# Optimization experiments

Hardware: AMD Instinct MI355X
Metric: run time of the kernel (lower is better)

Reference implementation:

```python
import jax, jax.numpy as jnp
import numpy as np

GROUP_SIZE = 128
TOP_K = 2
ZERO_POINT = 8  # Marlin symmetric zero point: w = scale * (q - 8)


def _dequant_int4(q, scales, group_size):
    # q: [E, N, K] int values in [0,15]; scales: [E, N, K//group_size]
    s = jnp.repeat(scales, group_size, axis=-1)  # [E, N, K]
    return (q.astype(jnp.float32) - float(ZERO_POINT)) * s


def setup_inputs() -> dict:
    key = jax.random.key(0)
    k1, k2, k3, k4, k5, k6 = jax.random.split(key, 6)
    B, S, H, I, E = 2, 1024, 2048, 1408, 8
    router_logits = jax.random.normal(k1, (B, S, E), dtype=jnp.float32)
    hidden_states = jax.random.normal(k2, (B, S, H), dtype=jnp.float32)
    fc_gate_up_qweights = jax.random.randint(k3, (E, 2 * I, H), 0, 16, dtype=jnp.int32)
    fc_gate_up_scales = jax.random.uniform(k4, (E, 2 * I, H // GROUP_SIZE), dtype=jnp.float32) * 0.02
    fc_down_qweights = jax.random.randint(k5, (E, H, I), 0, 16, dtype=jnp.int32)
    fc_down_scales = jax.random.uniform(k6, (E, H, I // GROUP_SIZE), dtype=jnp.float32) * 0.02
    return {
        "router_logits": router_logits,
        "hidden_states": hidden_states,
        "fc_gate_up_qweights": fc_gate_up_qweights,
        "fc_gate_up_scales": fc_gate_up_scales,
        "fc_down_qweights": fc_down_qweights,
        "fc_down_scales": fc_down_scales,
    }


def reference(router_logits, hidden_states, fc_gate_up_qweights, fc_gate_up_scales,
              fc_down_qweights, fc_down_scales):
    B, S, H = hidden_states.shape
    E = router_logits.shape[-1]
    T = B * S
    x = hidden_states.reshape(T, H)
    logits = router_logits.reshape(T, E)

    # top-k routing with softmax over selected logits
    top_vals, top_idx = jax.lax.top_k(logits, TOP_K)          # [T, k]
    top_w = jax.nn.softmax(top_vals, axis=-1)                 # [T, k]
    route_w = jnp.zeros((T, E), x.dtype).at[jnp.arange(T)[:, None], top_idx].set(top_w)  # [T, E]

    # dequantize int4 weights: scale * (q - 8), per-group along K
    w_gate_up = _dequant_int4(fc_gate_up_qweights, fc_gate_up_scales, GROUP_SIZE)  # [E, 2I, H]
    w_down = _dequant_int4(fc_down_qweights, fc_down_scales, GROUP_SIZE)          # [E, H, I]

    # grouped GEMM (dense over experts, masked by routing weights)
    gu = jnp.einsum('th,enh->ten', x, w_gate_up)              # [T, E, 2I]
    gate, up = jnp.split(gu, 2, axis=-1)
    act = jax.nn.silu(gate) * up                              # SwiGLU, [T, E, I]
    out = jnp.einsum('tei,ehi,te->th', act, w_down, route_w)  # [T, H]
    return out.reshape(B, S, H)
```

## Files before the change

### kernel.cpp

```cpp
#include <hip/hip_runtime.h>
#include <hip/hip_bf16.h>

#define T_TOKENS 2048
#define H_DIM    2048
#define I_DIM    1408
#define E_NUM    8

typedef __bf16 bf16;
typedef __attribute__((ext_vector_type(4))) __bf16  bf16x4;
typedef __attribute__((ext_vector_type(8))) __bf16  bf16x8;
typedef __attribute__((ext_vector_type(4))) float   floatx4;

static const size_t OFF_COUNTS = 0;
static const size_t OFF_LISTS  = 256;
static const size_t OFF_WLISTS = OFF_LISTS + (size_t)T_TOKENS * E_NUM * 4;
static const size_t OFF_ACT    = 262144;
static const size_t OFF_TMP    = OFF_ACT + (size_t)2 * T_TOKENS * I_DIM * 2;

__global__ void router_kernel(const float* __restrict__ logits,
                              int* __restrict__ counts,
                              int* __restrict__ lists,
                              float* __restrict__ wlists)
{
    int t = blockIdx.x * blockDim.x + threadIdx.x;
    if (t >= T_TOKENS) return;
    const float* l = logits + (size_t)t * E_NUM;
    float v0 = -1e30f, v1 = -1e30f;
    int i0 = 0, i1 = 0;
    #pragma unroll
    for (int e = 0; e < E_NUM; ++e) {
        float v = l[e];
        if (v > v0) { v1 = v0; i1 = i0; v0 = v; i0 = e; }
        else if (v > v1) { v1 = v; i1 = e; }
    }
    float w0 = 1.f / (1.f + __expf(v1 - v0));
    float w1 = 1.f - w0;
    int p0 = atomicAdd(&counts[i0], 1);
    lists[i0 * T_TOKENS + p0] = t * 2 + 0;
    wlists[i0 * T_TOKENS + p0] = w0;
    int p1 = atomicAdd(&counts[i1], 1);
    lists[i1 * T_TOKENS + p1] = t * 2 + 1;
    wlists[i1 * T_TOKENS + p1] = w1;
}

__global__ __launch_bounds__(256) void gemm1_kernel(
    const float* __restrict__ x,
    const int*   __restrict__ qw,
    const float* __restrict__ sc,
    const int*   __restrict__ counts,
    const int*   __restrict__ lists,
    bf16*        __restrict__ act)
{
    const int e   = blockIdx.z;
    const int cnt = counts[e];
    const int m0  = blockIdx.y * 128;
    if (m0 >= cnt) return;
    const int n0 = blockIdx.x * 64;

    __shared__ __align__(16) bf16 Al[128 * 64];
    __shared__ __align__(16) bf16 Bl[128 * 64];
    __shared__ int meta[128];

    const int tid = threadIdx.x;
    if (tid < 128) {
        int m = m0 + tid;
        meta[tid] = lists[e * T_TOKENS + (m < cnt ? m : 0)];
    }
    __syncthreads();

    const int lane = tid & 63;
    const int wv = tid >> 6;
    const int wm = wv >> 1, wn = wv & 1;

    floatx4 acc[4][4];
    #pragma unroll
    for (int i = 0; i < 4; ++i)
        #pragma unroll
        for (int j = 0; j < 4; ++j)
            acc[i][j] = (floatx4){0.f, 0.f, 0.f, 0.f};

    const int srow = tid >> 4;
    const int scol = (tid & 15) * 4;

    for (int k0 = 0; k0 < H_DIM; k0 += 64) {
        #pragma unroll
        for (int it = 0; it < 8; ++it) {
            int r = srow + 16 * it;
            int tok = meta[r] >> 1;
            float4 v = *reinterpret_cast<const float4*>(x + (size_t)tok * H_DIM + k0 + scol);
            bf16x4 bv; bv.x = (bf16)v.x; bv.y = (bf16)v.y; bv.z = (bf16)v.z; bv.w = (bf16)v.w;
            *reinterpret_cast<bf16x4*>(&Al[r * 64 + scol]) = bv;
        }
        #pragma unroll
        for (int it = 0; it < 8; ++it) {
            int r = srow + 16 * it;
            int tt = r >> 4, within = r & 15;
            int grow = ((tt & 1) ? I_DIM : 0) + n0 + (tt >> 1) * 16 + within;
            const int4 q = *reinterpret_cast<const int4*>(qw + (size_t)(e * 2816 + grow) * H_DIM + k0 + scol);
            float s = sc[(e * 2816 + grow) * 16 + (k0 >> 7)];
            bf16x4 bv;
            bv.x = (bf16)((float)(q.x - 8) * s);
            bv.y = (bf16)((float)(q.y - 8) * s);
            bv.z = (bf16)((float)(q.z - 8) * s);
            bv.w = (bf16)((float)(q.w - 8) * s);
            *reinterpret_cast<bf16x4*>(&Bl[r * 64 + scol]) = bv;
        }
        __syncthreads();
        #pragma unroll
        for (int ks = 0; ks < 2; ++ks) {
            const int kofs = ks * 32 + (lane >> 4) * 8;
            bf16x8 af[4], bfr[4];
            #pragma unroll
            for (int mt = 0; mt < 4; ++mt)
                af[mt] = *reinterpret_cast<const bf16x8*>(&Al[(wm * 64 + mt * 16 + (lane & 15)) * 64 + kofs]);
            #pragma unroll
            for (int nt = 0; nt < 4; ++nt)
                bfr[nt] = *reinterpret_cast<const bf16x8*>(&Bl[(wn * 64 + nt * 16 + (lane & 15)) * 64 + kofs]);
            #pragma unroll
            for (int mt = 0; mt < 4; ++mt)
                #pragma unroll
                for (int nt = 0; nt < 4; ++nt)
                    acc[mt][nt] = __builtin_amdgcn_mfma_f32_16x16x32_bf16(af[mt], bfr[nt], acc[mt][nt], 0, 0, 0);
        }
        __syncthreads();
    }

    const int rbase = (lane >> 4) * 4;
    const int cn = lane & 15;
    #pragma unroll
    for (int mt = 0; mt < 4; ++mt) {
        #pragma unroll
        for (int j = 0; j < 2; ++j) {
            floatx4 g = acc[mt][2 * j];
            floatx4 u = acc[mt][2 * j + 1];
            int col = n0 + wn * 32 + j * 16 + cn;
            #pragma unroll
            for (int r = 0; r < 4; ++r) {
                int lrow = wm * 64 + mt * 16 + rbase + r;
                if (m0 + lrow < cnt) {
                    float gate = g[r], up = u[r];
                    float a = gate / (1.f + __expf(-gate)) * up;
                    act[(size_t)meta[lrow] * I_DIM + col] = (bf16)a;
                }
            }
        }
    }
}

__global__ __launch_bounds__(256) void gemm2_kernel(
    const bf16*  __restrict__ act,
    const int*   __restrict__ qw,
    const float* __restrict__ sc,
    const int*   __restrict__ counts,
    const int*   __restrict__ lists,
    const float* __restrict__ wlists,
    float*       __restrict__ tmp)
{
    const int e   = blockIdx.z;
    const int cnt = counts[e];
    const int m0  = blockIdx.y * 128;
    if (m0 >= cnt) return;
    const int n0 = blockIdx.x * 128;

    __shared__ __align__(16) bf16 Al[128 * 64];
    __shared__ __align__(16) bf16 Bl[128 * 64];
    __shared__ int   meta[128];
    __shared__ float wmeta[128];

    const int tid = threadIdx.x;
    if (tid < 128) {
        int m = m0 + tid;
        int mm = (m < cnt) ? m : 0;
        meta[tid]  = lists[e * T_TOKENS + mm];
        wmeta[tid] = wlists[e * T_TOKENS + mm];
    }
    __syncthreads();

    const int lane = tid & 63;
    const int wv = tid >> 6;
    const int wm = wv >> 1, wn = wv & 1;

    floatx4 acc[4][4];
    #pragma unroll
    for (int i = 0; i < 4; ++i)
        #pragma unroll
        for (int j = 0; j < 4; ++j)
            acc[i][j] = (floatx4){0.f, 0.f, 0.f, 0.f};

    const int srow = tid >> 4;
    const int scol = (tid & 15) * 4;

    for (int k0 = 0; k0 < I_DIM; k0 += 64) {
        #pragma unroll
        for (int it = 0; it < 8; ++it) {
            int r = srow + 16 * it;
            bf16x4 v = *reinterpret_cast<const bf16x4*>(act + (size_t)meta[r] * I_DIM + k0 + scol);
            *reinterpret_cast<bf16x4*>(&Al[r * 64 + scol]) = v;
        }
        #pragma unroll
        for (int it = 0; it < 8; ++it) {
            int r = srow + 16 * it;
            int grow = n0 + r;
            const int4 q = *reinterpret_cast<const int4*>(qw + (size_t)(e * H_DIM + grow) * I_DIM + k0 + scol);
            float s = sc[(e * H_DIM + grow) * 11 + (k0 >> 7)];
            bf16x4 bv;
            bv.x = (bf16)((float)(q.x - 8) * s);
            bv.y = (bf16)((float)(q.y - 8) * s);
            bv.z = (bf16)((float)(q.z - 8) * s);
            bv.w = (bf16)((float)(q.w - 8) * s);
            *reinterpret_cast<bf16x4*>(&Bl[r * 64 + scol]) = bv;
        }
        __syncthreads();
        #pragma unroll
        for (int ks = 0; ks < 2; ++ks) {
            const int kofs = ks * 32 + (lane >> 4) * 8;
            bf16x8 af[4], bfr[4];
            #pragma unroll
            for (int mt = 0; mt < 4; ++mt)
                af[mt] = *reinterpret_cast<const bf16x8*>(&Al[(wm * 64 + mt * 16 + (lane & 15)) * 64 + kofs]);
            #pragma unroll
            for (int nt = 0; nt < 4; ++nt)
                bfr[nt] = *reinterpret_cast<const bf16x8*>(&Bl[(wn * 64 + nt * 16 + (lane & 15)) * 64 + kofs]);
            #pragma unroll
            for (int mt = 0; mt < 4; ++mt)
                #pragma unroll
                for (int nt = 0; nt < 4; ++nt)
                    acc[mt][nt] = __builtin_amdgcn_mfma_f32_16x16x32_bf16(af[mt], bfr[nt], acc[mt][nt], 0, 0, 0);
        }
        __syncthreads();
    }

    const int rbase = (lane >> 4) * 4;
    const int cn = lane & 15;
    #pragma unroll
    for (int mt = 0; mt < 4; ++mt) {
        #pragma unroll
        for (int nt = 0; nt < 4; ++nt) {
            floatx4 v = acc[mt][nt];
            int col = n0 + wn * 64 + nt * 16 + cn;
            #pragma unroll
            for (int r = 0; r < 4; ++r) {
                int lrow = wm * 64 + mt * 16 + rbase + r;
                if (m0 + lrow < cnt) {
                    tmp[(size_t)meta[lrow] * H_DIM + col] = wmeta[lrow] * v[r];
                }
            }
        }
    }
}

__global__ void finalize_kernel(const float* __restrict__ tmp, float* __restrict__ out)
{
    int i4 = blockIdx.x * blockDim.x + threadIdx.x;
    int t  = i4 >> 9;
    int h  = (i4 & 511) * 4;
    float4 a = *reinterpret_cast<const float4*>(tmp + ((size_t)2 * t) * H_DIM + h);
    float4 b = *reinterpret_cast<const float4*>(tmp + ((size_t)(2 * t + 1)) * H_DIM + h);
    float4 o;
    o.x = a.x + b.x; o.y = a.y + b.y; o.z = a.z + b.z; o.w = a.w + b.w;
    *reinterpret_cast<float4*>(out + (size_t)t * H_DIM + h) = o;
}

extern "C" void kernel_launch(void* const* d_in, const int* in_sizes, int n_in,
                              void* d_out, int out_size, void* d_ws, size_t ws_size,
                              hipStream_t stream)
{
    const float* router_logits = (const float*)d_in[0];
    const float* x             = (const float*)d_in[1];
    const int*   gu_q          = (const int*)d_in[2];
    const float* gu_s          = (const float*)d_in[3];
    const int*   dn_q          = (const int*)d_in[4];
    const float* dn_s          = (const float*)d_in[5];
    float* out = (float*)d_out;

    char* ws = (char*)d_ws;
    int*   counts = (int*)(ws + OFF_COUNTS);
    int*   lists  = (int*)(ws + OFF_LISTS);
    float* wlists = (float*)(ws + OFF_WLISTS);
    bf16*  act    = (bf16*)(ws + OFF_ACT);
    float* tmp    = (float*)(ws + OFF_TMP);

    hipMemsetAsync(counts, 0, E_NUM * sizeof(int), stream);
    router_kernel<<<T_TOKENS / 256, 256, 0, stream>>>(router_logits, counts, lists, wlists);
    gemm1_kernel<<<dim3(22, 16, 8), 256, 0, stream>>>(x, gu_q, gu_s, counts, lists, act);
    gemm2_kernel<<<dim3(16, 16, 8), 256, 0, stream>>>(act, dn_q, dn_s, counts, lists, wlists, tmp);
    finalize_kernel<<<4096, 256, 0, stream>>>(tmp, out);
}
```

Baseline: 559.6 us.

## Pre-pack int4 weights to nibbles, pre-convert x to bf16, atomic-add output

Adds per-call pre-pass kernels that pack the int32 quantized weights into 4-bit nibbles and convert hidden states to bf16. The GEMMs then load the packed words and dequantize them with an FMA per element, and load activations with wider 16-byte vector loads. The finalize kernel and tmp buffer are removed: gemm2 atomically adds weighted results straight into a zeroed output. The pack kernels still read all int32 weights every call, so total traffic may not drop, and the fp32 atomics make the summation order nondeterministic.

```diff
diff --git a/kernel.cpp b/kernel.cpp
--- a/kernel.cpp
+++ b/kernel.cpp
@@ -14,8 +14,38 @@
 static const size_t OFF_COUNTS = 0;
 static const size_t OFF_LISTS  = 256;
 static const size_t OFF_WLISTS = OFF_LISTS + (size_t)T_TOKENS * E_NUM * 4;
-static const size_t OFF_ACT    = 262144;
-static const size_t OFF_TMP    = OFF_ACT + (size_t)2 * T_TOKENS * I_DIM * 2;
+static const size_t OFF_XB     = 131328;
+static const size_t OFF_ACT    = OFF_XB + (size_t)T_TOKENS * H_DIM * 2;
+static const size_t OFF_GUPK   = OFF_ACT + (size_t)2 * T_TOKENS * I_DIM * 2;
+static const size_t OFF_DNPK   = OFF_GUPK + (size_t)E_NUM * 2 * I_DIM * (H_DIM / 8) * 4;
+
+__global__ void pack_nib_kernel(const int* __restrict__ q, uint2* __restrict__ out, int n2)
+{
+    int i = blockIdx.x * blockDim.x + threadIdx.x;
+    if (i >= n2) return;
+    const int4* q4 = reinterpret_cast<const int4*>(q) + (size_t)i * 4;
+    int4 a = q4[0], b = q4[1], c = q4[2], d = q4[3];
+    unsigned d0 = (unsigned)(a.x & 15) | ((unsigned)(a.y & 15) << 4) |
+                  ((unsigned)(a.z & 15) << 8) | ((unsigned)(a.w & 15) << 12) |
+                  ((unsigned)(b.x & 15) << 16) | ((unsigned)(b.y & 15) << 20) |
+                  ((unsigned)(b.z & 15) << 24) | ((unsigned)(b.w & 15) << 28);
+    unsigned d1 = (unsigned)(c.x & 15) | ((unsigned)(c.y & 15) << 4) |
+                  ((unsigned)(c.z & 15) << 8) | ((unsigned)(c.w & 15) << 12) |
+                  ((unsigned)(d.x & 15) << 16) | ((unsigned)(d.y & 15) << 20) |
+                  ((unsigned)(d.z & 15) << 24) | ((unsigned)(d.w & 15) << 28);
+    out[i] = make_uint2(d0, d1);
+}
+
+__global__ void xconv_kernel(const float* __restrict__ x, bf16* __restrict__ xb)
+{
+    int i = blockIdx.x * blockDim.x + threadIdx.x;
+    const float4* x4 = reinterpret_cast<const float4*>(x) + (size_t)i * 2;
+    float4 v0 = x4[0], v1 = x4[1];
+    bf16x8 bv;
+    bv[0] = (bf16)v0.x; bv[1] = (bf16)v0.y; bv[2] = (bf16)v0.z; bv[3] = (bf16)v0.w;
+    bv[4] = (bf16)v1.x; bv[5] = (bf16)v1.y; bv[6] = (bf16)v1.z; bv[7] = (bf16)v1.w;
+    *reinterpret_cast<bf16x8*>(xb + (size_t)i * 8) = bv;
+}
 
 __global__ void router_kernel(const float* __restrict__ logits,
                               int* __restrict__ counts,
@@ -44,12 +74,12 @@
 }
 
 __global__ __launch_bounds__(256) void gemm1_kernel(
-    const float* __restrict__ x,
-    const int*   __restrict__ qw,
-    const float* __restrict__ sc,
-    const int*   __restrict__ counts,
-    const int*   __restrict__ lists,
-    bf16*        __restrict__ act)
+    const bf16*     __restrict__ xb,
+    const unsigned* __restrict__ qpk,
+    const float*    __restrict__ sc,
+    const int*      __restrict__ counts,
+    const int*      __restrict__ lists,
+    bf16*           __restrict__ act)
 {
     const int e   = blockIdx.z;
     const int cnt = counts[e];
@@ -79,31 +109,32 @@
         for (int j = 0; j < 4; ++j)
             acc[i][j] = (floatx4){0.f, 0.f, 0.f, 0.f};
 
-    const int srow = tid >> 4;
-    const int scol = (tid & 15) * 4;
+    const int kg   = tid & 7;
+    const int rb   = tid >> 3;
 
     for (int k0 = 0; k0 < H_DIM; k0 += 64) {
         #pragma unroll
-        for (int it = 0; it < 8; ++it) {
-            int r = srow + 16 * it;
-            int tok = meta[r] >> 1;
-            float4 v = *reinterpret_cast<const float4*>(x + (size_t)tok * H_DIM + k0 + scol);
-            bf16x4 bv; bv.x = (bf16)v.x; bv.y = (bf16)v.y; bv.z = (bf16)v.z; bv.w = (bf16)v.w;
-            *reinterpret_cast<bf16x4*>(&Al[r * 64 + scol]) = bv;
-        }
-        #pragma unroll
-        for (int it = 0; it < 8; ++it) {
-            int r = srow + 16 * it;
+        for (int j = 0; j < 4; ++j) {
+            int g = tid + 256 * j;
+            int row = g >> 3, cg = g & 7;
+            int tok = meta[row] >> 1;
+            bf16x8 v = *reinterpret_cast<const bf16x8*>(xb + (size_t)tok * H_DIM + k0 + cg * 8);
+            *reinterpret_cast<bf16x8*>(&Al[g * 8]) = v;
+        }
+        #pragma unroll
+        for (int j = 0; j < 4; ++j) {
+            int r = rb + 32 * j;
             int tt = r >> 4, within = r & 15;
             int grow = ((tt & 1) ? I_DIM : 0) + n0 + (tt >> 1) * 16 + within;
-            const int4 q = *reinterpret_cast<const int4*>(qw + (size_t)(e * 2816 + grow) * H_DIM + k0 + scol);
-            float s = sc[(e * 2816 + grow) * 16 + (k0 >> 7)];
-            bf16x4 bv;
-            bv.x = (bf16)((float)(q.x - 8) * s);
-            bv.y = (bf16)((float)(q.y - 8) * s);
-            bv.z = (bf16)((float)(q.z - 8) * s);
-            bv.w = (bf16)((float)(q.w - 8) * s);
-            *reinterpret_cast<bf16x4*>(&Bl[r * 64 + scol]) = bv;
+            size_t rbase = (size_t)(e * 2816 + grow);
+            unsigned pd = qpk[rbase * 256 + (k0 >> 3) + kg];
+            float s = sc[rbase * 16 + (k0 >> 7)];
+            float m8s = -8.f * s;
+            bf16x8 bv;
+            #pragma unroll
+            for (int jj = 0; jj < 8; ++jj)
+                bv[jj] = (bf16)fmaf((float)((pd >> (4 * jj)) & 15u), s, m8s);
+            *reinterpret_cast<bf16x8*>(&Bl[r * 64 + kg * 8]) = bv;
         }
         __syncthreads();
         #pragma unroll
@@ -148,13 +179,13 @@
 }
 
 __global__ __launch_bounds__(256) void gemm2_kernel(
-    const bf16*  __restrict__ act,
-    const int*   __restrict__ qw,
-    const float* __restrict__ sc,
-    const int*   __restrict__ counts,
-    const int*   __restrict__ lists,
-    const float* __restrict__ wlists,
-    float*       __restrict__ tmp)
+    const bf16*     __restrict__ act,
+    const unsigned* __restrict__ qpk,
+    const float*    __restrict__ sc,
+    const int*      __restrict__ counts,
+    const int*      __restrict__ lists,
+    const float*    __restrict__ wlists,
+    float*          __restrict__ out)
 {
     const int e   = blockIdx.z;
     const int cnt = counts[e];
@@ -187,28 +218,30 @@
         for (int j = 0; j < 4; ++j)
             acc[i][j] = (floatx4){0.f, 0.f, 0.f, 0.f};
 
-    const int srow = tid >> 4;
-    const int scol = (tid & 15) * 4;
+    const int kg = tid & 7;
+    const int rb = tid >> 3;
 
     for (int k0 = 0; k0 < I_DIM; k0 += 64) {
         #pragma unroll
-        for (int it = 0; it < 8; ++it) {
-            int r = srow + 16 * it;
-            bf16x4 v = *reinterpret_cast<const bf16x4*>(act + (size_t)meta[r] * I_DIM + k0 + scol);
-            *reinterpret_cast<bf16x4*>(&Al[r * 64 + scol]) = v;
-        }
-        #pragma unroll
-        for (int it = 0; it < 8; ++it) {
-            int r = srow + 16 * it;
+        for (int j = 0; j < 4; ++j) {
+            int g = tid + 256 * j;
+            int row = g >> 3, cg = g & 7;
+            bf16x8 v = *reinterpret_cast<const bf16x8*>(act + (size_t)meta[row] * I_DIM + k0 + cg * 8);
+            *reinterpret_cast<bf16x8*>(&Al[g * 8]) = v;
+        }
+        #pragma unroll
+        for (int j = 0; j < 4; ++j) {
+            int r = rb + 32 * j;
             int grow = n0 + r;
-            const int4 q = *reinterpret_cast<const int4*>(qw + (size_t)(e * H_DIM + grow) * I_DIM + k0 + scol);
-            float s = sc[(e * H_DIM + grow) * 11 + (k0 >> 7)];
-            bf16x4 bv;
-            bv.x = (bf16)((float)(q.x - 8) * s);
-            bv.y = (bf16)((float)(q.y - 8) * s);
-            bv.z = (bf16)((float)(q.z - 8) * s);
-            bv.w = (bf16)((float)(q.w - 8) * s);
-            *reinterpret_cast<bf16x4*>(&Bl[r * 64 + scol]) = bv;
+            size_t rbase = (size_t)(e * H_DIM + grow);
+            unsigned pd = qpk[rbase * 176 + (k0 >> 3) + kg];
+            float s = sc[rbase * 11 + (k0 >> 7)];
+            float m8s = -8.f * s;
+            bf16x8 bv;
+            #pragma unroll
+            for (int jj = 0; jj < 8; ++jj)
+                bv[jj] = (bf16)fmaf((float)((pd >> (4 * jj)) & 15u), s, m8s);
+            *reinterpret_cast<bf16x8*>(&Bl[r * 64 + kg * 8]) = bv;
         }
         __syncthreads();
         #pragma unroll
@@ -242,23 +275,12 @@
             for (int r = 0; r < 4; ++r) {
                 int lrow = wm * 64 + mt * 16 + rbase + r;
                 if (m0 + lrow < cnt) {
-                    tmp[(size_t)meta[lrow] * H_DIM + col] = wmeta[lrow] * v[r];
+                    int tok = meta[lrow] >> 1;
+                    unsafeAtomicAdd(&out[(size_t)tok * H_DIM + col], wmeta[lrow] * v[r]);
                 }
             }
         }
     }
-}
-
-__global__ void finalize_kernel(const float* __restrict__ tmp, float* __restrict__ out)
-{
-    int i4 = blockIdx.x * blockDim.x + threadIdx.x;
-    int t  = i4 >> 9;
-    int h  = (i4 & 511) * 4;
-    float4 a = *reinterpret_cast<const float4*>(tmp + ((size_t)2 * t) * H_DIM + h);
-    float4 b = *reinterpret_cast<const float4*>(tmp + ((size_t)(2 * t + 1)) * H_DIM + h);
-    float4 o;
-    o.x = a.x + b.x; o.y = a.y + b.y; o.z = a.z + b.z; o.w = a.w + b.w;
-    *reinterpret_cast<float4*>(out + (size_t)t * H_DIM + h) = o;
 }
 
 extern "C" void kernel_launch(void* const* d_in, const int* in_sizes, int n_in,
@@ -274,15 +296,24 @@
     float* out = (float*)d_out;
 
     char* ws = (char*)d_ws;
-    int*   counts = (int*)(ws + OFF_COUNTS);
-    int*   lists  = (int*)(ws + OFF_LISTS);
-    float* wlists = (float*)(ws + OFF_WLISTS);
-    bf16*  act    = (bf16*)(ws + OFF_ACT);
-    float* tmp    = (float*)(ws + OFF_TMP);
+    int*      counts = (int*)(ws + OFF_COUNTS);
+    int*      lists  = (int*)(ws + OFF_LISTS);
+    float*    wlists = (float*)(ws + OFF_WLISTS);
+    bf16*     xb     = (bf16*)(ws + OFF_XB);
+    bf16*     act    = (bf16*)(ws + OFF_ACT);
+    unsigned* gu_pk  = (unsigned*)(ws + OFF_GUPK);
+    unsigned* dn_pk  = (unsigned*)(ws + OFF_DNPK);
 
     hipMemsetAsync(counts, 0, E_NUM * sizeof(int), stream);
+    hipMemsetAsync(out, 0, (size_t)out_size * sizeof(float), stream);
+
+    const int n2_gu = E_NUM * 2 * I_DIM * H_DIM / 16;
+    const int n2_dn = E_NUM * H_DIM * I_DIM / 16;
+    pack_nib_kernel<<<(n2_gu + 255) / 256, 256, 0, stream>>>(gu_q, (uint2*)gu_pk, n2_gu);
+    pack_nib_kernel<<<(n2_dn + 255) / 256, 256, 0, stream>>>(dn_q, (uint2*)dn_pk, n2_dn);
+    xconv_kernel<<<T_TOKENS * H_DIM / 8 / 256, 256, 0, stream>>>(x, xb);
+
     router_kernel<<<T_TOKENS / 256, 256, 0, stream>>>(router_logits, counts, lists, wlists);
-    gemm1_kernel<<<dim3(22, 16, 8), 256, 0, stream>>>(x, gu_q, gu_s, counts, lists, act);
-    gemm2_kernel<<<dim3(16, 16, 8), 256, 0, stream>>>(act, dn_q, dn_s, counts, lists, wlists, tmp);
-    finalize_kernel<<<4096, 256, 0, stream>>>(tmp, out);
-}
+    gemm1_kernel<<<dim3(22, 16, 8), 256, 0, stream>>>(xb, gu_pk, gu_s, counts, lists, act);
+    gemm2_kernel<<<dim3(16, 16, 8), 256, 0, stream>>>(act, dn_pk, dn_s, counts, lists, wlists, out);
+}
```

After: 568.7 us. About the same (+1.6%).

## Pre-dequantize weights into swizzled bf16 tiles and pre-convert activations

Applied to the files above, without the earlier changes.

Adds pack kernels that dequantize the int4-as-int32 weights once into bf16, laid out tile-contiguous with an XOR swizzle, plus a kernel that converts x to bf16. The GEMM kernels then do plain 16-byte copies into shared memory with conflict-free swizzled fragment reads. The aim is to stop re-reading fp32/int32 data and re-dequantizing it once per M-tile, and to cut LDS bank conflicts. The cost is extra full passes over the weights each call (read int32, write bf16) and a larger workspace, with tmp now overlapping the gate-up packed buffer.

```diff
diff --git a/kernel.cpp b/kernel.cpp
--- a/kernel.cpp
+++ b/kernel.cpp
@@ -7,15 +7,85 @@
 #define E_NUM    8
 
 typedef __bf16 bf16;
-typedef __attribute__((ext_vector_type(4))) __bf16  bf16x4;
 typedef __attribute__((ext_vector_type(8))) __bf16  bf16x8;
 typedef __attribute__((ext_vector_type(4))) float   floatx4;
 
 static const size_t OFF_COUNTS = 0;
 static const size_t OFF_LISTS  = 256;
 static const size_t OFF_WLISTS = OFF_LISTS + (size_t)T_TOKENS * E_NUM * 4;
-static const size_t OFF_ACT    = 262144;
-static const size_t OFF_TMP    = OFF_ACT + (size_t)2 * T_TOKENS * I_DIM * 2;
+static const size_t OFF_XB     = 131328;
+static const size_t OFF_ACT    = OFF_XB + (size_t)T_TOKENS * H_DIM * 2;
+static const size_t OFF_GUPK   = OFF_ACT + (size_t)2 * T_TOKENS * I_DIM * 2;
+static const size_t OFF_DNPK   = OFF_GUPK + (size_t)E_NUM * 22 * 32 * 16384;
+static const size_t OFF_TMP    = OFF_GUPK;
+
+__global__ __launch_bounds__(256) void pack_gu_kernel(const int* __restrict__ q,
+                                                      const float* __restrict__ sc,
+                                                      bf16* __restrict__ out)
+{
+    const int b = blockIdx.x;
+    const int t = threadIdx.x;
+    const int e = b / 2816;
+    const int grow = b - e * 2816;
+    const int4* qp = reinterpret_cast<const int4*>(q + (size_t)b * H_DIM) + t * 2;
+    int4 a = qp[0], c = qp[1];
+    float s = sc[(size_t)b * 16 + (t >> 4)];
+    float m8s = -8.f * s;
+    bf16x8 bv;
+    bv[0] = (bf16)fmaf((float)a.x, s, m8s);
+    bv[1] = (bf16)fmaf((float)a.y, s, m8s);
+    bv[2] = (bf16)fmaf((float)a.z, s, m8s);
+    bv[3] = (bf16)fmaf((float)a.w, s, m8s);
+    bv[4] = (bf16)fmaf((float)c.x, s, m8s);
+    bv[5] = (bf16)fmaf((float)c.y, s, m8s);
+    bv[6] = (bf16)fmaf((float)c.z, s, m8s);
+    bv[7] = (bf16)fmaf((float)c.w, s, m8s);
+    const int is_up = grow >= I_DIM;
+    const int icol  = grow - (is_up ? I_DIM : 0);
+    const int nt    = icol >> 6;
+    const int r     = ((((icol >> 4) & 3) * 2 + is_up) * 16) + (icol & 15);
+    size_t dst = ((((size_t)e * 22 + nt) * 32 + (t >> 3)) * 128 + r) * 8 + ((t & 7) ^ (r & 7));
+    reinterpret_cast<bf16x8*>(out)[dst] = bv;
+}
+
+__global__ __launch_bounds__(256) void pack_dn_kernel(const int* __restrict__ q,
+                                                      const float* __restrict__ sc,
+                                                      bf16* __restrict__ out)
+{
+    const int b = blockIdx.x;
+    const int t = threadIdx.x;
+    if (t >= 176) return;
+    const int e = b >> 11;
+    const int grow = b & 2047;
+    const int4* qp = reinterpret_cast<const int4*>(q + (size_t)b * I_DIM) + t * 2;
+    int4 a = qp[0], c = qp[1];
+    float s = sc[(size_t)b * 11 + (t >> 4)];
+    float m8s = -8.f * s;
+    bf16x8 bv;
+    bv[0] = (bf16)fmaf((float)a.x, s, m8s);
+    bv[1] = (bf16)fmaf((float)a.y, s, m8s);
+    bv[2] = (bf16)fmaf((float)a.z, s, m8s);
+    bv[3] = (bf16)fmaf((float)a.w, s, m8s);
+    bv[4] = (bf16)fmaf((float)c.x, s, m8s);
+    bv[5] = (bf16)fmaf((float)c.y, s, m8s);
+    bv[6] = (bf16)fmaf((float)c.z, s, m8s);
+    bv[7] = (bf16)fmaf((float)c.w, s, m8s);
+    const int nt = grow >> 7;
+    const int r  = grow & 127;
+    size_t dst = ((((size_t)e * 16 + nt) * 22 + (t >> 3)) * 128 + r) * 8 + ((t & 7) ^ (r & 7));
+    reinterpret_cast<bf16x8*>(out)[dst] = bv;
+}
+
+__global__ void xconv_kernel(const float* __restrict__ x, bf16* __restrict__ xb)
+{
+    int i = blockIdx.x * blockDim.x + threadIdx.x;
+    const float4* x4 = reinterpret_cast<const float4*>(x) + (size_t)i * 2;
+    float4 v0 = x4[0], v1 = x4[1];
+    bf16x8 bv;
+    bv[0] = (bf16)v0.x; bv[1] = (bf16)v0.y; bv[2] = (bf16)v0.z; bv[3] = (bf16)v0.w;
+    bv[4] = (bf16)v1.x; bv[5] = (bf16)v1.y; bv[6] = (bf16)v1.z; bv[7] = (bf16)v1.w;
+    *reinterpret_cast<bf16x8*>(xb + (size_t)i * 8) = bv;
+}
 
 __global__ void router_kernel(const float* __restrict__ logits,
                               int* __restrict__ counts,
@@ -44,21 +114,20 @@
 }
 
 __global__ __launch_bounds__(256) void gemm1_kernel(
-    const float* __restrict__ x,
-    const int*   __restrict__ qw,
-    const float* __restrict__ sc,
-    const int*   __restrict__ counts,
-    const int*   __restrict__ lists,
-    bf16*        __restrict__ act)
+    const bf16* __restrict__ xb,
+    const bf16* __restrict__ wpk,
+    const int*  __restrict__ counts,
+    const int*  __restrict__ lists,
+    bf16*       __restrict__ act)
 {
     const int e   = blockIdx.z;
     const int cnt = counts[e];
     const int m0  = blockIdx.y * 128;
     if (m0 >= cnt) return;
-    const int n0 = blockIdx.x * 64;
-
-    __shared__ __align__(16) bf16 Al[128 * 64];
-    __shared__ __align__(16) bf16 Bl[128 * 64];
+    const int nt  = blockIdx.x;
+
+    __shared__ __align__(16) bf16 Al[8192];
+    __shared__ __align__(16) bf16 Bl[8192];
     __shared__ int meta[128];
 
     const int tid = threadIdx.x;
@@ -72,6 +141,30 @@
     const int wv = tid >> 6;
     const int wm = wv >> 1, wn = wv & 1;
 
+    int    aoff[4];
+    size_t agbl[4];
+    #pragma unroll
+    for (int j = 0; j < 4; ++j) {
+        int g = tid + 256 * j;
+        int arow = g >> 3, cg = g & 7;
+        aoff[j] = arow * 64 + ((cg ^ (arow & 7)) * 8);
+        agbl[j] = (size_t)(meta[arow] >> 1) * H_DIM + cg * 8;
+    }
+    const bf16* bt = wpk + ((size_t)e * 22 + nt) * (32 * 8192) + tid * 8;
+
+    int afr[2][4], bfr[2][4];
+    #pragma unroll
+    for (int ks = 0; ks < 2; ++ks) {
+        int gidx = ks * 4 + (lane >> 4);
+        #pragma unroll
+        for (int t4 = 0; t4 < 4; ++t4) {
+            int ra = wm * 64 + t4 * 16 + (lane & 15);
+            afr[ks][t4] = ra * 64 + ((gidx ^ (ra & 7)) * 8);
+            int rb = wn * 64 + t4 * 16 + (lane & 15);
+            bfr[ks][t4] = rb * 64 + ((gidx ^ (rb & 7)) * 8);
+        }
+    }
+
     floatx4 acc[4][4];
     #pragma unroll
     for (int i = 0; i < 4; ++i)
@@ -79,48 +172,33 @@
         for (int j = 0; j < 4; ++j)
             acc[i][j] = (floatx4){0.f, 0.f, 0.f, 0.f};
 
-    const int srow = tid >> 4;
-    const int scol = (tid & 15) * 4;
-
     for (int k0 = 0; k0 < H_DIM; k0 += 64) {
         #pragma unroll
-        for (int it = 0; it < 8; ++it) {
-            int r = srow + 16 * it;
-            int tok = meta[r] >> 1;
-            float4 v = *reinterpret_cast<const float4*>(x + (size_t)tok * H_DIM + k0 + scol);
-            bf16x4 bv; bv.x = (bf16)v.x; bv.y = (bf16)v.y; bv.z = (bf16)v.z; bv.w = (bf16)v.w;
-            *reinterpret_cast<bf16x4*>(&Al[r * 64 + scol]) = bv;
-        }
-        #pragma unroll
-        for (int it = 0; it < 8; ++it) {
-            int r = srow + 16 * it;
-            int tt = r >> 4, within = r & 15;
-            int grow = ((tt & 1) ? I_DIM : 0) + n0 + (tt >> 1) * 16 + within;
-            const int4 q = *reinterpret_cast<const int4*>(qw + (size_t)(e * 2816 + grow) * H_DIM + k0 + scol);
-            float s = sc[(e * 2816 + grow) * 16 + (k0 >> 7)];
-            bf16x4 bv;
-            bv.x = (bf16)((float)(q.x - 8) * s);
-            bv.y = (bf16)((float)(q.y - 8) * s);
-            bv.z = (bf16)((float)(q.z - 8) * s);
-            bv.w = (bf16)((float)(q.w - 8) * s);
-            *reinterpret_cast<bf16x4*>(&Bl[r * 64 + scol]) = bv;
+        for (int j = 0; j < 4; ++j) {
+            bf16x8 v = *reinterpret_cast<const bf16x8*>(xb + agbl[j] + k0);
+            *reinterpret_cast<bf16x8*>(&Al[aoff[j]]) = v;
+        }
+        const bf16* bsrc = bt + (size_t)(k0 >> 6) * 8192;
+        #pragma unroll
+        for (int j = 0; j < 4; ++j) {
+            bf16x8 v = *reinterpret_cast<const bf16x8*>(bsrc + j * 2048);
+            *reinterpret_cast<bf16x8*>(&Bl[tid * 8 + j * 2048]) = v;
         }
         __syncthreads();
         #pragma unroll
         for (int ks = 0; ks < 2; ++ks) {
-            const int kofs = ks * 32 + (lane >> 4) * 8;
-            bf16x8 af[4], bfr[4];
+            bf16x8 af[4], bff[4];
             #pragma unroll
             for (int mt = 0; mt < 4; ++mt)
-                af[mt] = *reinterpret_cast<const bf16x8*>(&Al[(wm * 64 + mt * 16 + (lane & 15)) * 64 + kofs]);
-            #pragma unroll
-            for (int nt = 0; nt < 4; ++nt)
-                bfr[nt] = *reinterpret_cast<const bf16x8*>(&Bl[(wn * 64 + nt * 16 + (lane & 15)) * 64 + kofs]);
+                af[mt] = *reinterpret_cast<const bf16x8*>(&Al[afr[ks][mt]]);
+            #pragma unroll
+            for (int ntf = 0; ntf < 4; ++ntf)
+                bff[ntf] = *reinterpret_cast<const bf16x8*>(&Bl[bfr[ks][ntf]]);
             #pragma unroll
             for (int mt = 0; mt < 4; ++mt)
                 #pragma unroll
-                for (int nt = 0; nt < 4; ++nt)
-                    acc[mt][nt] = __builtin_amdgcn_mfma_f32_16x16x32_bf16(af[mt], bfr[nt], acc[mt][nt], 0, 0, 0);
+                for (int ntf = 0; ntf < 4; ++ntf)
+                    acc[mt][ntf] = __builtin_amdgcn_mfma_f32_16x16x32_bf16(af[mt], bff[ntf], acc[mt][ntf], 0, 0, 0);
         }
         __syncthreads();
     }
@@ -133,7 +211,7 @@
         for (int j = 0; j < 2; ++j) {
             floatx4 g = acc[mt][2 * j];
             floatx4 u = acc[mt][2 * j + 1];
-            int col = n0 + wn * 32 + j * 16 + cn;
+            int col = nt * 64 + (wn * 2 + j) * 16 + cn;
             #pragma unroll
             for (int r = 0; r < 4; ++r) {
                 int lrow = wm * 64 + mt * 16 + rbase + r;
@@ -149,8 +227,7 @@
 
 __global__ __launch_bounds__(256) void gemm2_kernel(
     const bf16*  __restrict__ act,
-    const int*   __restrict__ qw,
-    const float* __restrict__ sc,
+    const bf16*  __restrict__ wpk,
     const int*   __restrict__ counts,
     const int*   __restrict__ lists,
     const float* __restrict__ wlists,
@@ -160,10 +237,10 @@
     const int cnt = counts[e];
     const int m0  = blockIdx.y * 128;
     if (m0 >= cnt) return;
-    const int n0 = blockIdx.x * 128;
-
-    __shared__ __align__(16) bf16 Al[128 * 64];
-    __shared__ __align__(16) bf16 Bl[128 * 64];
+    const int nt  = blockIdx.x;
+
+    __shared__ __align__(16) bf16 Al[8192];
+    __shared__ __align__(16) bf16 Bl[8192];
     __shared__ int   meta[128];
     __shared__ float wmeta[128];
 
@@ -180,6 +257,30 @@
     const int wv = tid >> 6;
     const int wm = wv >> 1, wn = wv & 1;
 
+    int    aoff[4];
+    size_t agbl[4];
+    #pragma unroll
+    for (int j = 0; j < 4; ++j) {
+        int g = tid + 256 * j;
+        int arow = g >> 3, cg = g & 7;
+        aoff[j] = arow * 64 + ((cg ^ (arow & 7)) * 8);
+        agbl[j] = (size_t)meta[arow] * I_DIM + cg * 8;
+    }
+    const bf16* bt = wpk + ((size_t)e * 16 + nt) * (22 * 8192) + tid * 8;
+
+    int afr[2][4], bfr[2][4];
+    #pragma unroll
+    for (int ks = 0; ks < 2; ++ks) {
+        int gidx = ks * 4 + (lane >> 4);
+        #pragma unroll
+        for (int t4 = 0; t4 < 4; ++t4) {
+            int ra = wm * 64 + t4 * 16 + (lane & 15);
+            afr[ks][t4] = ra * 64 + ((gidx ^ (ra & 7)) * 8);
+            int rb = wn * 64 + t4 * 16 + (lane & 15);
+            bfr[ks][t4] = rb * 64 + ((gidx ^ (rb & 7)) * 8);
+        }
+    }
+
     floatx4 acc[4][4];
     #pragma unroll
     for (int i = 0; i < 4; ++i)
@@ -187,45 +288,33 @@
         for (int j = 0; j < 4; ++j)
             acc[i][j] = (floatx4){0.f, 0.f, 0.f, 0.f};
 
-    const int srow = tid >> 4;
-    const int scol = (tid & 15) * 4;
-
-    for (int k0 = 0; k0 < I_DIM; k0 += 64) {
-        #pragma unroll
-        for (int it = 0; it < 8; ++it) {
-            int r = srow + 16 * it;
-            bf16x4 v = *reinterpret_cast<const bf16x4*>(act + (size_t)meta[r] * I_DIM + k0 + scol);
-            *reinterpret_cast<bf16x4*>(&Al[r * 64 + scol]) = v;
-        }
-        #pragma unroll
-        for (int it = 0; it < 8; ++it) {
-            int r = srow + 16 * it;
-            int grow = n0 + r;
-            const int4 q = *reinterpret_cast<const int4*>(qw + (size_t)(e * H_DIM + grow) * I_DIM + k0 + scol);
-            float s = sc[(e * H_DIM + grow) * 11 + (k0 >> 7)];
-            bf16x4 bv;
-            bv.x = (bf16)((float)(q.x - 8) * s);
-            bv.y = (bf16)((float)(q.y - 8) * s);
-            bv.z = (bf16)((float)(q.z - 8) * s);
-            bv.w = (bf16)((float)(q.w - 8) * s);
-            *reinterpret_cast<bf16x4*>(&Bl[r * 64 + scol]) = bv;
+    for (int kt = 0; kt < 22; ++kt) {
+        #pragma unroll
+        for (int j = 0; j < 4; ++j) {
+            bf16x8 v = *reinterpret_cast<const bf16x8*>(act + agbl[j] + kt * 64);
+            *reinterpret_cast<bf16x8*>(&Al[aoff[j]]) = v;
+        }
+        const bf16* bsrc = bt + (size_t)kt * 8192;
+        #pragma unroll
+        for (int j = 0; j < 4; ++j) {
+            bf16x8 v = *reinterpret_cast<const bf16x8*>(bsrc + j * 2048);
+            *reinterpret_cast<bf16x8*>(&Bl[tid * 8 + j * 2048]) = v;
         }
         __syncthreads();
         #pragma unroll
         for (int ks = 0; ks < 2; ++ks) {
-            const int kofs = ks * 32 + (lane >> 4) * 8;
-            bf16x8 af[4], bfr[4];
+            bf16x8 af[4], bff[4];
             #pragma unroll
             for (int mt = 0; mt < 4; ++mt)
-                af[mt] = *reinterpret_cast<const bf16x8*>(&Al[(wm * 64 + mt * 16 + (lane & 15)) * 64 + kofs]);
-            #pragma unroll
-            for (int nt = 0; nt < 4; ++nt)
-                bfr[nt] = *reinterpret_cast<const bf16x8*>(&Bl[(wn * 64 + nt * 16 + (lane & 15)) * 64 + kofs]);
+                af[mt] = *reinterpret_cast<const bf16x8*>(&Al[afr[ks][mt]]);
+            #pragma unroll
+            for (int ntf = 0; ntf < 4; ++ntf)
+                bff[ntf] = *reinterpret_cast<const bf16x8*>(&Bl[bfr[ks][ntf]]);
             #pragma unroll
             for (int mt = 0; mt < 4; ++mt)
                 #pragma unroll
-                for (int nt = 0; nt < 4; ++nt)
-                    acc[mt][nt] = __builtin_amdgcn_mfma_f32_16x16x32_bf16(af[mt], bfr[nt], acc[mt][nt], 0, 0, 0);
+                for (int ntf = 0; ntf < 4; ++ntf)
+                    acc[mt][ntf] = __builtin_amdgcn_mfma_f32_16x16x32_bf16(af[mt], bff[ntf], acc[mt][ntf], 0, 0, 0);
         }
         __syncthreads();
     }
@@ -235,9 +324,9 @@
     #pragma unroll
     for (int mt = 0; mt < 4; ++mt) {
         #pragma unroll
-        for (int nt = 0; nt < 4; ++nt) {
-            floatx4 v = acc[mt][nt];
-            int col = n0 + wn * 64 + nt * 16 + cn;
+        for (int ntf = 0; ntf < 4; ++ntf) {
+            floatx4 v = acc[mt][ntf];
+            int col = nt * 128 + wn * 64 + ntf * 16 + cn;
             #pragma unroll
             for (int r = 0; r < 4; ++r) {
                 int lrow = wm * 64 + mt * 16 + rbase + r;
@@ -277,12 +366,20 @@
     int*   counts = (int*)(ws + OFF_COUNTS);
     int*   lists  = (int*)(ws + OFF_LISTS);
     float* wlists = (float*)(ws + OFF_WLISTS);
+    bf16*  xb     = (bf16*)(ws + OFF_XB);
     bf16*  act    = (bf16*)(ws + OFF_ACT);
+    bf16*  gu_pk  = (bf16*)(ws + OFF_GUPK);
+    bf16*  dn_pk  = (bf16*)(ws + OFF_DNPK);
     float* tmp    = (float*)(ws + OFF_TMP);
 
     hipMemsetAsync(counts, 0, E_NUM * sizeof(int), stream);
+
+    pack_gu_kernel<<<E_NUM * 2816, 256, 0, stream>>>(gu_q, gu_s, gu_pk);
+    pack_dn_kernel<<<E_NUM * 2048, 256, 0, stream>>>(dn_q, dn_s, dn_pk);
+    xconv_kernel<<<T_TOKENS * H_DIM / 8 / 256, 256, 0, stream>>>(x, xb);
     router_kernel<<<T_TOKENS / 256, 256, 0, stream>>>(router_logits, counts, lists, wlists);
-    gemm1_kernel<<<dim3(22, 16, 8), 256, 0, stream>>>(x, gu_q, gu_s, counts, lists, act);
-    gemm2_kernel<<<dim3(16, 16, 8), 256, 0, stream>>>(act, dn_q, dn_s, counts, lists, wlists, tmp);
+
+    gemm1_kernel<<<dim3(22, 16, 8), 256, 0, stream>>>(xb, gu_pk, counts, lists, act);
+    gemm2_kernel<<<dim3(16, 16, 8), 256, 0, stream>>>(act, dn_pk, counts, lists, wlists, tmp);
     finalize_kernel<<<4096, 256, 0, stream>>>(tmp, out);
 }
```

After: 522.2 us. 1.07x faster.
